# Kernel optimization log

Hardware: AMD Instinct MI355X
Metric: run time of the kernel (lower is better)

## Reference

```python
import jax, jax.numpy as jnp
import numpy as np


def setup_inputs() -> dict:
    key = jax.random.key(0)
    ks = jax.random.split(key, 7)
    B, S, D, H, Dh = 4, 2048, 1024, 16, 64
    return {
        "query_input": jax.random.normal(ks[0], (B, S, D), jnp.float32),
        "key_input": jax.random.normal(ks[1], (B, S, D), jnp.float32),
        "value_input": jax.random.normal(ks[2], (B, S, D), jnp.float32),
        "Wq": jax.random.normal(ks[3], (D, H, Dh), jnp.float32) * 0.03,
        "Wk": jax.random.normal(ks[4], (D, H, Dh), jnp.float32) * 0.03,
        "Wv": jax.random.normal(ks[5], (D, H, Dh), jnp.float32) * 0.03,
        "Wo": jax.random.normal(ks[6], (H, Dh, D), jnp.float32) * 0.03,
    }


def reference(query_input, key_input, value_input, Wq, Wk, Wv, Wo):
    # Projections: [B,S,D] x [D,H,Dh] -> [B,S,H,Dh]
    q = jnp.einsum("bsd,dhk->bshk", query_input, Wq)
    k = jnp.einsum("bsd,dhk->bshk", key_input, Wk)
    v = jnp.einsum("bsd,dhk->bshk", value_input, Wv)
    depth = Wq.shape[-1]
    q = q * (depth ** -0.5)
    # logits: [B,H,F,T]  (F = query len, T = key len)
    logits = jnp.einsum("bthk,bfhk->bhft", k, q)
    weights = jax.nn.softmax(logits, axis=-1)
    # attention output: [B,F,H,Dh]
    ctx = jnp.einsum("bhft,bthk->bfhk", weights, v)
    # output projection: [B,F,H,Dh] x [H,Dh,D] -> [B,F,D]
    return jnp.einsum("bfhk,hkd->bfd", ctx, Wo)
```

## Files before the change

kernel.cpp:

```cpp
#include <hip/hip_runtime.h>
#include <stdint.h>

typedef __bf16 bf16;
typedef __bf16 bf16x4 __attribute__((ext_vector_type(4)));
typedef __bf16 bf16x8 __attribute__((ext_vector_type(8)));
typedef float f32x4 __attribute__((ext_vector_type(4)));

#define AS1 __attribute__((address_space(1)))
#define AS3 __attribute__((address_space(3)))

__device__ __forceinline__ void async16(void* lds, const void* g) {
    __builtin_amdgcn_global_load_lds((AS1 void*)g, (AS3 void*)lds, 16, 0, 0);
}

__global__ __launch_bounds__(256) void prep(
    const float* __restrict__ x0, const float* __restrict__ x1,
    const float* __restrict__ x2,
    bf16* __restrict__ y0, bf16* __restrict__ y1, bf16* __restrict__ y2,
    const float* __restrict__ s0, const float* __restrict__ s1,
    const float* __restrict__ s2, const float* __restrict__ s3,
    bf16* __restrict__ d0, bf16* __restrict__ d1,
    bf16* __restrict__ d2, bf16* __restrict__ d3) {
    const int z = blockIdx.z;
    const int t = threadIdx.x;
    if (z < 3) {
        const float* x = z == 0 ? x0 : z == 1 ? x1 : x2;
        bf16* y = z == 0 ? y0 : z == 1 ? y1 : y2;
        int i = (blockIdx.x * 256 + t) * 8;
        f32x4 a = *(const f32x4*)(x + i);
        f32x4 b = *(const f32x4*)(x + i + 4);
        bf16x8 o;
#pragma unroll
        for (int j = 0; j < 4; ++j) { o[j] = (bf16)a[j]; o[4 + j] = (bf16)b[j]; }
        *(bf16x8*)(y + i) = o;
        return;
    }
    const int bx = blockIdx.x;
    if (bx >= 1024) return;
    const int wsel = bx >> 8, tile = bx & 255;
    const float* W = wsel == 0 ? s0 : wsel == 1 ? s1 : wsel == 2 ? s2 : s3;
    bf16* Wt = wsel == 0 ? d0 : wsel == 1 ? d1 : wsel == 2 ? d2 : d3;
    const int k0 = (tile >> 4) * 64, n0 = (tile & 15) * 64;
    __shared__ float Ts[64 * 65];
    const int c = t & 63, r0 = t >> 6;
#pragma unroll
    for (int i = 0; i < 16; ++i) {
        int r = r0 + i * 4;
        Ts[r * 65 + c] = W[(size_t)(k0 + r) * 1024 + n0 + c];
    }
    __syncthreads();
#pragma unroll
    for (int i = 0; i < 16; ++i) {
        int r = r0 + i * 4;
        Wt[(size_t)(n0 + r) * 1024 + k0 + c] = (bf16)Ts[c * 65 + r];
    }
}

template <typename OutT>
__device__ __forceinline__ void gemm_body(const bf16* __restrict__ A,
                                          const bf16* __restrict__ Bt,
                                          OutT* __restrict__ C,
                                          int N, int K, float scale,
                                          int m0, int n0,
                                          bf16* As, bf16* Bs) {
    const int t = threadIdx.x;
    const int lane = t & 63;
    const int w = t >> 6;
    const int l15 = lane & 15;
    const int quad = lane >> 4;
    const int wm = w >> 1, wn = w & 1;

    f32x4 acc[4][4];
#pragma unroll
    for (int i = 0; i < 4; ++i)
#pragma unroll
        for (int j = 0; j < 4; ++j) acc[i][j] = (f32x4){0.f, 0.f, 0.f, 0.f};

    const bf16* gA[4];
    const bf16* gB[4];
#pragma unroll
    for (int j = 0; j < 4; ++j) {
        int c = j * 256 + t;
        int row = c >> 3, g = (c & 7) ^ (row & 7);
        gA[j] = A + (size_t)(m0 + row) * K + g * 8;
        gB[j] = Bt + (size_t)(n0 + row) * K + g * 8;
    }

    for (int k0 = 0; k0 < K; k0 += 64) {
        __syncthreads();
#pragma unroll
        for (int j = 0; j < 4; ++j) {
            async16(As + (j * 256 + w * 64) * 8, gA[j] + k0);
            async16(Bs + (j * 256 + w * 64) * 8, gB[j] + k0);
        }
        __syncthreads();
#pragma unroll
        for (int kk = 0; kk < 2; ++kk) {
            bf16x8 af[4], bfv[4];
#pragma unroll
            for (int mi = 0; mi < 4; ++mi) {
                int r = wm * 64 + mi * 16 + l15;
                af[mi] = *(const bf16x8*)&As[r * 64 + (((kk * 4 + quad) ^ (r & 7)) * 8)];
            }
#pragma unroll
            for (int ni = 0; ni < 4; ++ni) {
                int r = wn * 64 + ni * 16 + l15;
                bfv[ni] = *(const bf16x8*)&Bs[r * 64 + (((kk * 4 + quad) ^ (r & 7)) * 8)];
            }
#pragma unroll
            for (int mi = 0; mi < 4; ++mi)
#pragma unroll
                for (int ni = 0; ni < 4; ++ni)
                    acc[mi][ni] = __builtin_amdgcn_mfma_f32_16x16x32_bf16(
                        af[mi], bfv[ni], acc[mi][ni], 0, 0, 0);
        }
    }

#pragma unroll
    for (int mi = 0; mi < 4; ++mi)
#pragma unroll
        for (int ni = 0; ni < 4; ++ni)
#pragma unroll
            for (int r = 0; r < 4; ++r) {
                int row = m0 + wm * 64 + mi * 16 + quad * 4 + r;
                int col = n0 + wn * 64 + ni * 16 + l15;
                C[(size_t)row * N + col] = (OutT)(acc[mi][ni][r] * scale);
            }
}

__global__ __launch_bounds__(256) void gemm_qkv(
    const bf16* __restrict__ Xq, const bf16* __restrict__ Xk, const bf16* __restrict__ Xv,
    const bf16* __restrict__ Wqt, const bf16* __restrict__ Wkt, const bf16* __restrict__ Wvt,
    bf16* __restrict__ Qb, bf16* __restrict__ Kb, bf16* __restrict__ VtG) {
    __shared__ __align__(16) bf16 As[128 * 64];
    __shared__ __align__(16) bf16 Bs[128 * 64];
    const int z = blockIdx.z;
    const int blk = blockIdx.x;
    const bf16* A; const bf16* Bt; bf16* C; int N; float scale; int m0, n0;
    if (z == 0) { A = Xq; Bt = Wqt; C = Qb; N = 1024; scale = 0.125f;
                  m0 = (blk >> 3) * 128; n0 = (blk & 7) * 128; }
    else if (z == 1) { A = Xk; Bt = Wkt; C = Kb; N = 1024; scale = 1.0f;
                  m0 = (blk >> 3) * 128; n0 = (blk & 7) * 128; }
    else { A = Wvt; Bt = Xv; C = VtG; N = 8192; scale = 1.0f;
                  m0 = (blk >> 6) * 128; n0 = (blk & 63) * 128; }
    gemm_body<bf16>(A, Bt, C, N, 1024, scale, m0, n0, As, Bs);
}

__global__ __launch_bounds__(256) void gemm_out(const bf16* __restrict__ A,
                                                const bf16* __restrict__ Bt,
                                                float* __restrict__ C) {
    __shared__ __align__(16) bf16 As[128 * 64];
    __shared__ __align__(16) bf16 Bs[128 * 64];
    gemm_body<float>(A, Bt, C, 1024, 1024, 1.0f, blockIdx.y * 128, blockIdx.x * 128,
                     As, Bs);
}

__global__ __launch_bounds__(256) void attn_fa(const bf16* __restrict__ Q,
                                               const bf16* __restrict__ K,
                                               const bf16* __restrict__ Vt,
                                               bf16* __restrict__ O) {
    __shared__ __align__(16) bf16 Ks[2][64 * 64];
    __shared__ __align__(16) bf16 Vs[2][64 * 64];
    __shared__ __align__(16) bf16 Pt[4][32 * 72];

    const int t = threadIdx.x;
    const int lane = t & 63;
    const int w = t >> 6;
    const int l15 = lane & 15;
    const int quad = lane >> 4;
    const int bh = blockIdx.y;
    const int b = bh >> 4, h = bh & 15;
    const int q0 = blockIdx.x * 128;
    const size_t baseQ = (size_t)b * 2048 * 1024 + (size_t)h * 64;
    const float L2E = 1.44269504088896340736f;

    const int r0s = t >> 3,          g0s = (t & 7) ^ (r0s & 7);
    const int r1s = (t + 256) >> 3,  g1s = ((t + 256) & 7) ^ (r1s & 7);
    const bf16* gK0 = K + baseQ + (size_t)r0s * 1024 + g0s * 8;
    const bf16* gK1 = K + baseQ + (size_t)r1s * 1024 + g1s * 8;
    const bf16* gV0 = Vt + (size_t)(h * 64 + r0s) * 8192 + (size_t)b * 2048 + g0s * 8;
    const bf16* gV1 = Vt + (size_t)(h * 64 + r1s) * 8192 + (size_t)b * 2048 + g1s * 8;

    bf16x8 qf[2][2];
#pragma unroll
    for (int mi = 0; mi < 2; ++mi)
#pragma unroll
        for (int kk = 0; kk < 2; ++kk)
            qf[mi][kk] = *(const bf16x8*)(Q + baseQ +
                (size_t)(q0 + w * 32 + mi * 16 + l15) * 1024 + kk * 32 + quad * 8);

    f32x4 accO[4][2];
    float l_part[2] = {0.f, 0.f};
#pragma unroll
    for (int nd = 0; nd < 4; ++nd)
#pragma unroll
        for (int mi = 0; mi < 2; ++mi) accO[nd][mi] = (f32x4){0.f, 0.f, 0.f, 0.f};

    auto swz = [&](int r, int g) { return (r * 8 + (g ^ (r & 7))) * 8; };
    auto stage = [&](int t0, int bi) {
        async16((bf16*)Ks[bi] + w * 512,        gK0 + (size_t)t0 * 1024);
        async16((bf16*)Ks[bi] + 2048 + w * 512, gK1 + (size_t)t0 * 1024);
        async16((bf16*)Vs[bi] + w * 512,        gV0 + t0);
        async16((bf16*)Vs[bi] + 2048 + w * 512, gV1 + t0);
    };

    stage(0, 0);

    for (int it = 0; it < 32; ++it) {
        __syncthreads();
        if (it + 1 < 32) stage((it + 1) * 64, (it + 1) & 1);
        const bf16* Kb = Ks[it & 1];
        const bf16* Vb = Vs[it & 1];

        f32x4 accS[4][2];
#pragma unroll
        for (int nt = 0; nt < 4; ++nt)
#pragma unroll
            for (int mi = 0; mi < 2; ++mi) accS[nt][mi] = (f32x4){0.f, 0.f, 0.f, 0.f};
#pragma unroll
        for (int kk = 0; kk < 2; ++kk) {
            bf16x8 kf[4];
#pragma unroll
            for (int nt = 0; nt < 4; ++nt)
                kf[nt] = *(const bf16x8*)&Kb[swz(nt * 16 + l15, kk * 4 + quad)];
#pragma unroll
            for (int nt = 0; nt < 4; ++nt)
#pragma unroll
                for (int mi = 0; mi < 2; ++mi)
                    accS[nt][mi] = __builtin_amdgcn_mfma_f32_16x16x32_bf16(
                        kf[nt], qf[mi][kk], accS[nt][mi], 0, 0, 0);
        }

        bf16* Pp = &Pt[w][0];
#pragma unroll
        for (int mi = 0; mi < 2; ++mi) {
            float rs = 0.f;
#pragma unroll
            for (int nt = 0; nt < 4; ++nt) {
                bf16x4 pk;
#pragma unroll
                for (int r = 0; r < 4; ++r) {
                    float p = __builtin_amdgcn_exp2f(accS[nt][mi][r] * L2E);
                    rs += p;
                    pk[r] = (bf16)p;
                }
                *(bf16x4*)&Pp[(mi * 16 + l15) * 72 + nt * 16 + quad * 4] = pk;
            }
            l_part[mi] += rs;
        }

#pragma unroll
        for (int kk = 0; kk < 2; ++kk) {
            bf16x8 vf[4], pf[2];
#pragma unroll
            for (int nd = 0; nd < 4; ++nd)
                vf[nd] = *(const bf16x8*)&Vb[swz(nd * 16 + l15, kk * 4 + quad)];
#pragma unroll
            for (int mi = 0; mi < 2; ++mi)
                pf[mi] = *(const bf16x8*)&Pp[(mi * 16 + l15) * 72 + kk * 32 + quad * 8];
#pragma unroll
            for (int nd = 0; nd < 4; ++nd)
#pragma unroll
                for (int mi = 0; mi < 2; ++mi)
                    accO[nd][mi] = __builtin_amdgcn_mfma_f32_16x16x32_bf16(
                        vf[nd], pf[mi], accO[nd][mi], 0, 0, 0);
        }
    }

    float inv[2];
#pragma unroll
    for (int mi = 0; mi < 2; ++mi) {
        float l = l_part[mi];
        l += __shfl_xor(l, 16);
        l += __shfl_xor(l, 32);
        inv[mi] = 1.0f / l;
    }

#pragma unroll
    for (int mi = 0; mi < 2; ++mi) {
        size_t rowoff = baseQ + (size_t)(q0 + w * 32 + mi * 16 + l15) * 1024;
#pragma unroll
        for (int nd = 0; nd < 4; ++nd) {
            bf16x4 o;
#pragma unroll
            for (int r = 0; r < 4; ++r) o[r] = (bf16)(accO[nd][mi][r] * inv[mi]);
            *(bf16x4*)&O[rowoff + nd * 16 + quad * 4] = o;
        }
    }
}

extern "C" void kernel_launch(void* const* d_in, const int* in_sizes, int n_in,
                              void* d_out, int out_size, void* d_ws, size_t ws_size,
                              hipStream_t stream) {
    const float* qin = (const float*)d_in[0];
    const float* kin = (const float*)d_in[1];
    const float* vin = (const float*)d_in[2];
    const float* Wq = (const float*)d_in[3];
    const float* Wk = (const float*)d_in[4];
    const float* Wv = (const float*)d_in[5];
    const float* Wo = (const float*)d_in[6];
    float* out = (float*)d_out;

    char* ws = (char*)d_ws;
    bf16* Xq  = (bf16*)(ws);
    bf16* Xk  = (bf16*)(ws + ((size_t)16 << 20));
    bf16* Xv  = (bf16*)(ws + ((size_t)32 << 20));
    bf16* Qb  = (bf16*)(ws + ((size_t)48 << 20));
    bf16* Kb  = (bf16*)(ws + ((size_t)64 << 20));
    bf16* VtG = (bf16*)(ws + ((size_t)80 << 20));
    bf16* Cb  = (bf16*)(ws);
    bf16* Wqt = (bf16*)(ws + ((size_t)96 << 20));
    bf16* Wkt = Wqt + 1024 * 1024;
    bf16* Wvt = Wkt + 1024 * 1024;
    bf16* Wot = Wvt + 1024 * 1024;

    prep<<<dim3(4096, 1, 4), 256, 0, stream>>>(qin, kin, vin, Xq, Xk, Xv,
                                               Wq, Wk, Wv, Wo, Wqt, Wkt, Wvt, Wot);
    gemm_qkv<<<dim3(512, 1, 3), 256, 0, stream>>>(Xq, Xk, Xv, Wqt, Wkt, Wvt,
                                                  Qb, Kb, VtG);
    attn_fa<<<dim3(16, 64), 256, 0, stream>>>(Qb, Kb, VtG, Cb);
    gemm_out<<<dim3(8, 64), 256, 0, stream>>>(Cb, Wot, out);
}
```

Measured before the change: 345.7 us.

## Enlarge attention blocks to 512 threads, swizzle P tile, remap block order

Attention blocks now cover 256 query rows with 8 waves, so each staged K/V tile serves twice as many queries and each thread issues one async load per tile instead of two. The padded P buffer is replaced with an XOR-swizzled layout that avoids bank conflicts. log2(e) is folded into the Q projection scale so the exp2 needs no multiply. MFMA sections are wrapped in s_setprio, and the GEMM and attention grids are remapped so consecutive blocks share inputs in cache. The larger block raises register and LDS pressure per workgroup, which may lower occupancy.

```diff
diff --git a/kernel.cpp b/kernel.cpp
--- a/kernel.cpp
+++ b/kernel.cpp
@@ -136,13 +136,15 @@
     __shared__ __align__(16) bf16 Bs[128 * 64];
     const int z = blockIdx.z;
     const int blk = blockIdx.x;
+    const int big  = (blk & 7) * 8 + (blk >> 6);
+    const int sml  = (blk >> 3) & 7;
     const bf16* A; const bf16* Bt; bf16* C; int N; float scale; int m0, n0;
-    if (z == 0) { A = Xq; Bt = Wqt; C = Qb; N = 1024; scale = 0.125f;
-                  m0 = (blk >> 3) * 128; n0 = (blk & 7) * 128; }
+    if (z == 0) { A = Xq; Bt = Wqt; C = Qb; N = 1024; scale = 0.18033688011112042f;
+                  m0 = big * 128; n0 = sml * 128; }
     else if (z == 1) { A = Xk; Bt = Wkt; C = Kb; N = 1024; scale = 1.0f;
-                  m0 = (blk >> 3) * 128; n0 = (blk & 7) * 128; }
+                  m0 = big * 128; n0 = sml * 128; }
     else { A = Wvt; Bt = Xv; C = VtG; N = 8192; scale = 1.0f;
-                  m0 = (blk >> 6) * 128; n0 = (blk & 63) * 128; }
+                  m0 = sml * 128; n0 = big * 128; }
     gemm_body<bf16>(A, Bt, C, N, 1024, scale, m0, n0, As, Bs);
 }
 
@@ -151,35 +153,36 @@
                                                 float* __restrict__ C) {
     __shared__ __align__(16) bf16 As[128 * 64];
     __shared__ __align__(16) bf16 Bs[128 * 64];
-    gemm_body<float>(A, Bt, C, 1024, 1024, 1.0f, blockIdx.y * 128, blockIdx.x * 128,
-                     As, Bs);
-}
-
-__global__ __launch_bounds__(256) void attn_fa(const bf16* __restrict__ Q,
+    const int blk = blockIdx.x;
+    const int big = (blk & 7) * 8 + (blk >> 6);
+    const int sml = (blk >> 3) & 7;
+    gemm_body<float>(A, Bt, C, 1024, 1024, 1.0f, big * 128, sml * 128, As, Bs);
+}
+
+__global__ __launch_bounds__(512) void attn_fa(const bf16* __restrict__ Q,
                                                const bf16* __restrict__ K,
                                                const bf16* __restrict__ Vt,
                                                bf16* __restrict__ O) {
     __shared__ __align__(16) bf16 Ks[2][64 * 64];
     __shared__ __align__(16) bf16 Vs[2][64 * 64];
-    __shared__ __align__(16) bf16 Pt[4][32 * 72];
+    __shared__ __align__(16) bf16 Pt[8][32 * 64];
 
     const int t = threadIdx.x;
     const int lane = t & 63;
     const int w = t >> 6;
     const int l15 = lane & 15;
     const int quad = lane >> 4;
-    const int bh = blockIdx.y;
+    const int q7 = l15 & 7;
+
+    const int bid = blockIdx.x;
+    const int bh = (bid & 7) * 8 + ((bid >> 3) & 7);
+    const int q0 = (bid >> 6) * 256;
     const int b = bh >> 4, h = bh & 15;
-    const int q0 = blockIdx.x * 128;
     const size_t baseQ = (size_t)b * 2048 * 1024 + (size_t)h * 64;
-    const float L2E = 1.44269504088896340736f;
-
-    const int r0s = t >> 3,          g0s = (t & 7) ^ (r0s & 7);
-    const int r1s = (t + 256) >> 3,  g1s = ((t + 256) & 7) ^ (r1s & 7);
+
+    const int r0s = t >> 3, g0s = (t & 7) ^ (r0s & 7);
     const bf16* gK0 = K + baseQ + (size_t)r0s * 1024 + g0s * 8;
-    const bf16* gK1 = K + baseQ + (size_t)r1s * 1024 + g1s * 8;
     const bf16* gV0 = Vt + (size_t)(h * 64 + r0s) * 8192 + (size_t)b * 2048 + g0s * 8;
-    const bf16* gV1 = Vt + (size_t)(h * 64 + r1s) * 8192 + (size_t)b * 2048 + g1s * 8;
 
     bf16x8 qf[2][2];
 #pragma unroll
@@ -198,10 +201,8 @@
 
     auto swz = [&](int r, int g) { return (r * 8 + (g ^ (r & 7))) * 8; };
     auto stage = [&](int t0, int bi) {
-        async16((bf16*)Ks[bi] + w * 512,        gK0 + (size_t)t0 * 1024);
-        async16((bf16*)Ks[bi] + 2048 + w * 512, gK1 + (size_t)t0 * 1024);
-        async16((bf16*)Vs[bi] + w * 512,        gV0 + t0);
-        async16((bf16*)Vs[bi] + 2048 + w * 512, gV1 + t0);
+        async16((bf16*)Ks[bi] + w * 512, gK0 + (size_t)t0 * 1024);
+        async16((bf16*)Vs[bi] + w * 512, gV0 + t0);
     };
 
     stage(0, 0);
@@ -223,28 +224,32 @@
 #pragma unroll
             for (int nt = 0; nt < 4; ++nt)
                 kf[nt] = *(const bf16x8*)&Kb[swz(nt * 16 + l15, kk * 4 + quad)];
+            __builtin_amdgcn_s_setprio(1);
 #pragma unroll
             for (int nt = 0; nt < 4; ++nt)
 #pragma unroll
                 for (int mi = 0; mi < 2; ++mi)
                     accS[nt][mi] = __builtin_amdgcn_mfma_f32_16x16x32_bf16(
                         kf[nt], qf[mi][kk], accS[nt][mi], 0, 0, 0);
+            __builtin_amdgcn_s_setprio(0);
         }
 
         bf16* Pp = &Pt[w][0];
 #pragma unroll
         for (int mi = 0; mi < 2; ++mi) {
+            const int qbase = (mi * 16 + l15) * 64;
             float rs = 0.f;
 #pragma unroll
             for (int nt = 0; nt < 4; ++nt) {
                 bf16x4 pk;
 #pragma unroll
                 for (int r = 0; r < 4; ++r) {
-                    float p = __builtin_amdgcn_exp2f(accS[nt][mi][r] * L2E);
+                    float p = __builtin_amdgcn_exp2f(accS[nt][mi][r]);
                     rs += p;
                     pk[r] = (bf16)p;
                 }
-                *(bf16x4*)&Pp[(mi * 16 + l15) * 72 + nt * 16 + quad * 4] = pk;
+                *(bf16x4*)&Pp[qbase + (((nt * 2 + (quad >> 1)) ^ q7) * 8) +
+                              (quad & 1) * 4] = pk;
             }
             l_part[mi] += rs;
         }
@@ -257,13 +262,16 @@
                 vf[nd] = *(const bf16x8*)&Vb[swz(nd * 16 + l15, kk * 4 + quad)];
 #pragma unroll
             for (int mi = 0; mi < 2; ++mi)
-                pf[mi] = *(const bf16x8*)&Pp[(mi * 16 + l15) * 72 + kk * 32 + quad * 8];
+                pf[mi] = *(const bf16x8*)&Pp[(mi * 16 + l15) * 64 +
+                                             (((kk * 4 + quad) ^ q7) * 8)];
+            __builtin_amdgcn_s_setprio(1);
 #pragma unroll
             for (int nd = 0; nd < 4; ++nd)
 #pragma unroll
                 for (int mi = 0; mi < 2; ++mi)
                     accO[nd][mi] = __builtin_amdgcn_mfma_f32_16x16x32_bf16(
                         vf[nd], pf[mi], accO[nd][mi], 0, 0, 0);
+            __builtin_amdgcn_s_setprio(0);
         }
     }
 
@@ -318,6 +326,6 @@
                                                Wq, Wk, Wv, Wo, Wqt, Wkt, Wvt, Wot);
     gemm_qkv<<<dim3(512, 1, 3), 256, 0, stream>>>(Xq, Xk, Xv, Wqt, Wkt, Wvt,
                                                   Qb, Kb, VtG);
-    attn_fa<<<dim3(16, 64), 256, 0, stream>>>(Qb, Kb, VtG, Cb);
-    gemm_out<<<dim3(8, 64), 256, 0, stream>>>(Cb, Wot, out);
-}
+    attn_fa<<<dim3(512), 512, 0, stream>>>(Qb, Kb, VtG, Cb);
+    gemm_out<<<dim3(512), 256, 0, stream>>>(Cb, Wot, out);
+}
```

Result: faster. 312.6 us (median of 2 runs) (-9.6%).
